# Optimization experiments

Measured on AMD Instinct MI355X. Metric: run time of the kernel, lower is better.

Reference implementation:

```python
import jax, jax.numpy as jnp
import numpy as np

D_MODEL = 1024
NUM_HEADS = 16
D_K = D_MODEL // NUM_HEADS


def setup_inputs() -> dict:
    key = jax.random.key(0)
    ks = jax.random.split(key, 9)
    s = 1.0 / np.sqrt(D_MODEL)
    inp = {
        'x': jax.random.normal(ks[0], (1, 4096, D_MODEL), dtype=jnp.float32),
        'W_q': jax.random.uniform(ks[1], (D_MODEL, D_MODEL), jnp.float32, -s, s),
        'b_q': jax.random.uniform(ks[2], (D_MODEL,), jnp.float32, -s, s),
        'W_k': jax.random.uniform(ks[3], (D_MODEL, D_MODEL), jnp.float32, -s, s),
        'b_k': jax.random.uniform(ks[4], (D_MODEL,), jnp.float32, -s, s),
        'W_v': jax.random.uniform(ks[5], (D_MODEL, D_MODEL), jnp.float32, -s, s),
        'b_v': jax.random.uniform(ks[6], (D_MODEL,), jnp.float32, -s, s),
        'W_o': jax.random.uniform(ks[7], (D_MODEL, D_MODEL), jnp.float32, -s, s),
        'b_o': jax.random.uniform(ks[8], (D_MODEL,), jnp.float32, -s, s),
    }
    return inp


def reference(x, W_q, b_q, W_k, b_k, W_v, b_v, W_o, b_o):
    B, S, _ = x.shape
    def split_heads(t):  # [B,S,D] -> [B,H,S,d_k]
        return t.reshape(B, S, NUM_HEADS, D_K).transpose(0, 2, 1, 3)
    Q = split_heads(x @ W_q + b_q)
    K = split_heads(x @ W_k + b_k)
    V = split_heads(x @ W_v + b_v)
    scale = 1.0 / jnp.sqrt(jnp.float32(D_K))
    scores = jnp.einsum('bhqd,bhkd->bhqk', Q, K) * scale  # [B,H,S,S]
    attn = jax.nn.softmax(scores, axis=-1)
    ctx = jnp.einsum('bhqk,bhkd->bhqd', attn, V)
    ctx = ctx.transpose(0, 2, 1, 3).reshape(B, S, D_MODEL)
    return ctx @ W_o + b_o
```

## Files before the change

kernel.cpp:

```cpp
#include <hip/hip_runtime.h>
#include <hip/hip_bf16.h>
#include <stdint.h>


#define DM 1024
#define SEQ 4096
#define NH 16
#define DK 64

#define QSCALE 0.18033688011112042f

typedef __attribute__((ext_vector_type(8))) short bf16x8;
typedef __attribute__((ext_vector_type(4))) float f32x4;

__device__ __forceinline__ short f2bf(float f) {
  union { float f; uint32_t u; } x; x.f = f;
  uint32_t r = x.u + 0x7fffu + ((x.u >> 16) & 1u);
  return (short)(r >> 16);
}

__device__ __forceinline__ void gl_lds16(const void* g, void* l) {
  __builtin_amdgcn_global_load_lds(
      (const __attribute__((address_space(1))) void*)g,
      (__attribute__((address_space(3))) void*)l, 16, 0, 0);
}

__global__ __launch_bounds__(256) void cvt_x_k(const float* __restrict__ in,
                                               short* __restrict__ out) {
  size_t i = (size_t)blockIdx.x * 256 + threadIdx.x;
  const float4* ip = (const float4*)in;
  float4 a = ip[2 * i], b = ip[2 * i + 1];
  bf16x8 o;
  o[0] = f2bf(a.x); o[1] = f2bf(a.y); o[2] = f2bf(a.z); o[3] = f2bf(a.w);
  o[4] = f2bf(b.x); o[5] = f2bf(b.y); o[6] = f2bf(b.z); o[7] = f2bf(b.w);
  *(bf16x8*)(out + 8 * i) = o;
}

__global__ __launch_bounds__(256) void cvt_wt_k(const float* __restrict__ W0,
                                                const float* __restrict__ W1,
                                                const float* __restrict__ W2,
                                                const float* __restrict__ W3,
                                                short* __restrict__ Wt0) {
  __shared__ alignas(16) short T[64][66];
  const int z = blockIdx.z;
  const float* W = (z == 0) ? W0 : (z == 1) ? W1 : (z == 2) ? W2 : W3;
  short* Wt = Wt0 + (size_t)z * (DM * DM);
  const int k0 = blockIdx.y * 64, n0 = blockIdx.x * 64;
#pragma unroll
  for (int rep = 0; rep < 16; ++rep) {
    int lin = rep * 256 + threadIdx.x;
    int i = lin >> 6, j = lin & 63;
    T[i][j] = f2bf(W[(size_t)(k0 + i) * DM + n0 + j]);
  }
  __syncthreads();
#pragma unroll
  for (int rep = 0; rep < 16; ++rep) {
    int lin = rep * 256 + threadIdx.x;
    int n = lin >> 6, kk = lin & 63;
    Wt[(size_t)(n0 + n) * DM + k0 + kk] = T[kk][n];
  }
}

__global__ __launch_bounds__(256) void trans_v_k(const short* __restrict__ V,
                                                 short* __restrict__ Vt) {
  __shared__ alignas(16) short T[64][66];
  const int s0 = blockIdx.x * 64, h = blockIdx.y;
#pragma unroll
  for (int rep = 0; rep < 16; ++rep) {
    int lin = rep * 256 + threadIdx.x;
    int i = lin >> 6, j = lin & 63;
    T[i][j] = V[(size_t)(s0 + i) * DM + h * DK + j];
  }
  __syncthreads();
#pragma unroll
  for (int rep = 0; rep < 16; ++rep) {
    int lin = rep * 256 + threadIdx.x;
    int d = lin >> 6, ss = lin & 63;
    Vt[((size_t)h * DK + d) * SEQ + s0 + ss] = T[ss][d];
  }
}

__global__ __launch_bounds__(256) void gemm_qkv(
    const short* __restrict__ xb, const short* __restrict__ Wt0,
    const float* __restrict__ bq, const float* __restrict__ bk,
    const float* __restrict__ bv, short* __restrict__ out0) {
  const int z = blockIdx.z;
  const short* Bt = Wt0 + (size_t)z * (DM * DM);
  const float* bias = (z == 0) ? bq : (z == 1) ? bk : bv;
  const float qs = (z == 0) ? QSCALE : 1.0f;
  short* out = out0 + (size_t)z * ((size_t)SEQ * DM);

  __shared__ alignas(16) short As[128 * 32];
  __shared__ alignas(16) short Bs[128 * 32];
  const int tid = threadIdx.x, lane = tid & 63, w = tid >> 6;
  const int bm = blockIdx.y * 128, bn = blockIdx.x * 128;
  const int wm = (w >> 1) * 64, wn = (w & 1) * 64;
  f32x4 acc[4][4] = {};

  for (int kt = 0; kt < DM; kt += 32) {
    __syncthreads();
#pragma unroll
    for (int c = 0; c < 2; ++c) {
      int i = w * 2 + c;
      int ob = i * 1024 + lane * 16;
      int row = ob >> 6, colb = ob & 63;
      gl_lds16((const char*)xb + ((size_t)(bm + row) * DM + kt) * 2 + colb,
               (char*)As + i * 1024);
      gl_lds16((const char*)Bt + ((size_t)(bn + row) * DM + kt) * 2 + colb,
               (char*)Bs + i * 1024);
    }
    __syncthreads();
    bf16x8 bfr[4];
#pragma unroll
    for (int n = 0; n < 4; ++n)
      bfr[n] = *(const bf16x8*)((const char*)Bs +
                                (wn + n * 16 + (lane & 15)) * 64 + (lane >> 4) * 16);
#pragma unroll
    for (int m = 0; m < 4; ++m) {
      bf16x8 af = *(const bf16x8*)((const char*)As +
                                   (wm + m * 16 + (lane & 15)) * 64 + (lane >> 4) * 16);
#pragma unroll
      for (int n = 0; n < 4; ++n)
        acc[m][n] = __builtin_amdgcn_mfma_f32_16x16x32_bf16(af, bfr[n], acc[m][n], 0, 0, 0);
    }
  }
  const int r0 = bm + wm + ((lane >> 4) << 2);
  const int c0 = bn + wn + (lane & 15);
#pragma unroll
  for (int n = 0; n < 4; ++n) {
    const int col = c0 + n * 16;
    const float b = bias[col];
#pragma unroll
    for (int m = 0; m < 4; ++m)
#pragma unroll
      for (int r = 0; r < 4; ++r)
        out[(size_t)(r0 + m * 16 + r) * DM + col] = f2bf((acc[m][n][r] + b) * qs);
  }
}

__global__ __launch_bounds__(256) void gemm_out(
    const short* __restrict__ A, const short* __restrict__ Bt,
    const float* __restrict__ bias, float* __restrict__ out) {
  __shared__ alignas(16) short As[128 * 32];
  __shared__ alignas(16) short Bs[128 * 32];
  const int tid = threadIdx.x, lane = tid & 63, w = tid >> 6;
  const int bm = blockIdx.y * 128, bn = blockIdx.x * 128;
  const int wm = (w >> 1) * 64, wn = (w & 1) * 64;
  f32x4 acc[4][4] = {};

  for (int kt = 0; kt < DM; kt += 32) {
    __syncthreads();
#pragma unroll
    for (int c = 0; c < 2; ++c) {
      int i = w * 2 + c;
      int ob = i * 1024 + lane * 16;
      int row = ob >> 6, colb = ob & 63;
      gl_lds16((const char*)A + ((size_t)(bm + row) * DM + kt) * 2 + colb,
               (char*)As + i * 1024);
      gl_lds16((const char*)Bt + ((size_t)(bn + row) * DM + kt) * 2 + colb,
               (char*)Bs + i * 1024);
    }
    __syncthreads();
    bf16x8 bfr[4];
#pragma unroll
    for (int n = 0; n < 4; ++n)
      bfr[n] = *(const bf16x8*)((const char*)Bs +
                                (wn + n * 16 + (lane & 15)) * 64 + (lane >> 4) * 16);
#pragma unroll
    for (int m = 0; m < 4; ++m) {
      bf16x8 af = *(const bf16x8*)((const char*)As +
                                   (wm + m * 16 + (lane & 15)) * 64 + (lane >> 4) * 16);
#pragma unroll
      for (int n = 0; n < 4; ++n)
        acc[m][n] = __builtin_amdgcn_mfma_f32_16x16x32_bf16(af, bfr[n], acc[m][n], 0, 0, 0);
    }
  }
  const int r0 = bm + wm + ((lane >> 4) << 2);
  const int c0 = bn + wn + (lane & 15);
#pragma unroll
  for (int n = 0; n < 4; ++n) {
    const int col = c0 + n * 16;
    const float b = bias[col];
#pragma unroll
    for (int m = 0; m < 4; ++m)
#pragma unroll
      for (int r = 0; r < 4; ++r)
        out[(size_t)(r0 + m * 16 + r) * DM + col] = acc[m][n][r] + b;
  }
}

__global__ __launch_bounds__(256) void attn_k(
    const short* __restrict__ Qb, const short* __restrict__ Kb,
    const short* __restrict__ Vt, short* __restrict__ ctx) {
  const int h = blockIdx.y, qt = blockIdx.x;
  const int tid = threadIdx.x, lane = tid & 63, w = tid >> 6;
  __shared__ alignas(16) short Ks[64 * 64];
  __shared__ alignas(16) short Vs[64 * 64];
  __shared__ alignas(16) short Pl[4][16 * 64];

  const int qr = qt * 64 + w * 16 + (lane & 15);
  const short* qp = Qb + (size_t)qr * DM + h * DK + ((lane >> 4) * 8);
  const bf16x8 qf0 = *(const bf16x8*)qp;
  const bf16x8 qf1 = *(const bf16x8*)(qp + 32);

  bf16x8 ones;
#pragma unroll
  for (int j = 0; j < 8; ++j) ones[j] = (short)0x3F80;

  f32x4 o[4] = {};
  f32x4 ol = {};
  float mr[4];
#pragma unroll
  for (int r = 0; r < 4; ++r) mr[r] = -1e30f;

  const int xk = (lane & 7) << 4;
  char* pbase = (char*)&Pl[w][0];
  const int q2 = (lane & 15) * 2;

  for (int s0 = 0; s0 < SEQ; s0 += 64) {
    __syncthreads();
#pragma unroll
    for (int c = 0; c < 2; ++c) {
      int i = w * 2 + c;
      int ob = i * 1024 + lane * 16;
      int row = ob >> 7, colb = ob & 127;
      int src = colb ^ ((row & 7) << 4);
      gl_lds16((const char*)Kb + ((size_t)(s0 + row) * DM + h * DK) * 2 + src,
               (char*)Ks + i * 1024);
      gl_lds16((const char*)Vt + ((size_t)(h * DK + row) * SEQ + s0) * 2 + src,
               (char*)Vs + i * 1024);
    }
    __syncthreads();

    f32x4 sc[4] = {};
    __builtin_amdgcn_s_setprio(1);
#pragma unroll
    for (int kk = 0; kk < 2; ++kk) {
      bf16x8 a = kk ? qf1 : qf0;
#pragma unroll
      for (int n = 0; n < 4; ++n) {
        bf16x8 b = *(const bf16x8*)((const char*)Ks + (n * 16 + (lane & 15)) * 128 +
                                    ((kk * 64 + (lane >> 4) * 16) ^ xk));
        sc[n] = __builtin_amdgcn_mfma_f32_16x16x32_bf16(a, b, sc[n], 0, 0, 0);
      }
    }
    __builtin_amdgcn_s_setprio(0);

    float mx[4];
#pragma unroll
    for (int r = 0; r < 4; ++r) {
      float m = fmaxf(fmaxf(sc[0][r], sc[1][r]), fmaxf(sc[2][r], sc[3][r]));
      m = fmaxf(m, __shfl_xor(m, 1));
      m = fmaxf(m, __shfl_xor(m, 2));
      m = fmaxf(m, __shfl_xor(m, 4));
      m = fmaxf(m, __shfl_xor(m, 8));
      mx[r] = m;
    }
    bool ok = (mx[0] <= mr[0] + 8.f) & (mx[1] <= mr[1] + 8.f) &
              (mx[2] <= mr[2] + 8.f) & (mx[3] <= mr[3] + 8.f);
    if (!__all(ok)) {
#pragma unroll
      for (int r = 0; r < 4; ++r) {
        float mnew = fmaxf(mr[r], mx[r]);
        float alpha = exp2f(mr[r] - mnew);
        mr[r] = mnew;
        o[0][r] *= alpha; o[1][r] *= alpha; o[2][r] *= alpha; o[3][r] *= alpha;
        ol[r] *= alpha;
      }
    }
#pragma unroll
    for (int r = 0; r < 4; ++r) {
      const int prow = (lane >> 4) * 4 + r;
      char* pr = pbase + prow * 128;
      const int X = (prow & 7) << 4;
#pragma unroll
      for (int n = 0; n < 4; ++n) {
        float p = exp2f(sc[n][r] - mr[r]);
        *(short*)(pr + ((n * 32 + q2) ^ X)) = f2bf(p);
      }
    }

    __builtin_amdgcn_s_setprio(1);
#pragma unroll
    for (int kk = 0; kk < 2; ++kk) {
      bf16x8 pa = *(const bf16x8*)(pbase + (lane & 15) * 128 +
                                   ((kk * 64 + (lane >> 4) * 16) ^ xk));
      ol = __builtin_amdgcn_mfma_f32_16x16x32_bf16(pa, ones, ol, 0, 0, 0);
#pragma unroll
      for (int n = 0; n < 4; ++n) {
        bf16x8 vb = *(const bf16x8*)((const char*)Vs + (n * 16 + (lane & 15)) * 128 +
                                     ((kk * 64 + (lane >> 4) * 16) ^ xk));
        o[n] = __builtin_amdgcn_mfma_f32_16x16x32_bf16(pa, vb, o[n], 0, 0, 0);
      }
    }
    __builtin_amdgcn_s_setprio(0);
  }

#pragma unroll
  for (int r = 0; r < 4; ++r) {
    float inv = 1.f / ol[r];
    int row = qt * 64 + w * 16 + (lane >> 4) * 4 + r;
#pragma unroll
    for (int n = 0; n < 4; ++n)
      ctx[(size_t)row * DM + h * DK + n * 16 + (lane & 15)] = f2bf(o[n][r] * inv);
  }
}

extern "C" void kernel_launch(void* const* d_in, const int* in_sizes, int n_in,
                              void* d_out, int out_size, void* d_ws, size_t ws_size,
                              hipStream_t stream) {
  const float* x  = (const float*)d_in[0];
  const float* Wq = (const float*)d_in[1];
  const float* bq = (const float*)d_in[2];
  const float* Wk = (const float*)d_in[3];
  const float* bk = (const float*)d_in[4];
  const float* Wv = (const float*)d_in[5];
  const float* bv = (const float*)d_in[6];
  const float* Wo = (const float*)d_in[7];
  const float* bo = (const float*)d_in[8];

  char* ws = (char*)d_ws;
  short* xb  = (short*)(ws + (size_t)0);
  short* Wt  = (short*)(ws + ((size_t)8 << 20));
  short* Qb  = (short*)(ws + ((size_t)16 << 20));
  short* Kb  = (short*)(ws + ((size_t)24 << 20));
  short* Vb  = (short*)(ws + ((size_t)32 << 20));
  short* Vt  = (short*)(ws + ((size_t)40 << 20));
  short* ctx = (short*)(ws + ((size_t)48 << 20));
  (void)Vb;

  cvt_x_k<<<2048, 256, 0, stream>>>(x, xb);
  cvt_wt_k<<<dim3(16, 16, 4), 256, 0, stream>>>(Wq, Wk, Wv, Wo, Wt);
  gemm_qkv<<<dim3(DM / 128, SEQ / 128, 3), 256, 0, stream>>>(xb, Wt, bq, bk, bv, Qb);
  trans_v_k<<<dim3(SEQ / 64, NH), 256, 0, stream>>>(Vb, Vt);
  attn_k<<<dim3(SEQ / 64, NH), 256, 0, stream>>>(Qb, Kb, Vt, ctx);
  gemm_out<<<dim3(DM / 128, SEQ / 128), 256, 0, stream>>>(
      ctx, Wt + (size_t)3 * (DM * DM), bo, (float*)d_out);
}
```

Measured before the change: 326.7 us.

## Double-buffer K/V tiles, pack P stores, use a single per-wave running max

The attention kernel now double-buffers the K and V tiles in LDS, issuing the next tile's global-to-LDS loads before computing on the current one, and drops one barrier per iteration. V is stored transposed with a permuted sequence order so each lane can write four probabilities at once as packed bf16 (v_cvt_pk_bf16_f32) in a single 8-byte LDS store instead of four scalar stores. The online softmax keeps one running max per wave rather than per row, which cuts the shuffle reductions. The shared max is still exact after the final normalization, but rows whose scores sit far below the wave max could underflow in exp2. Doubling the K/V buffers also raises LDS use, which may lower occupancy.

```diff
diff --git a/kernel.cpp b/kernel.cpp
--- a/kernel.cpp
+++ b/kernel.cpp
@@ -12,6 +12,7 @@
 
 typedef __attribute__((ext_vector_type(8))) short bf16x8;
 typedef __attribute__((ext_vector_type(4))) float f32x4;
+typedef __attribute__((ext_vector_type(2))) uint32_t u32x2;
 
 __device__ __forceinline__ short f2bf(float f) {
   union { float f; uint32_t u; } x; x.f = f;
@@ -76,7 +77,8 @@
   for (int rep = 0; rep < 16; ++rep) {
     int lin = rep * 256 + threadIdx.x;
     int d = lin >> 6, ss = lin & 63;
-    Vt[((size_t)h * DK + d) * SEQ + s0 + ss] = T[ss][d];
+    int sp = ((ss & 15) << 2) + (ss >> 4);
+    Vt[((size_t)h * DK + d) * SEQ + s0 + sp] = T[ss][d];
   }
 }
 
@@ -194,8 +196,8 @@
     const short* __restrict__ Vt, short* __restrict__ ctx) {
   const int h = blockIdx.y, qt = blockIdx.x;
   const int tid = threadIdx.x, lane = tid & 63, w = tid >> 6;
-  __shared__ alignas(16) short Ks[64 * 64];
-  __shared__ alignas(16) short Vs[64 * 64];
+  __shared__ alignas(16) short Ks[2][64 * 64];
+  __shared__ alignas(16) short Vs[2][64 * 64];
   __shared__ alignas(16) short Pl[4][16 * 64];
 
   const int qr = qt * 64 + w * 16 + (lane & 15);
@@ -209,16 +211,13 @@
 
   f32x4 o[4] = {};
   f32x4 ol = {};
-  float mr[4];
-#pragma unroll
-  for (int r = 0; r < 4; ++r) mr[r] = -1e30f;
+  float m = -3000.f;
 
   const int xk = (lane & 7) << 4;
   char* pbase = (char*)&Pl[w][0];
-  const int q2 = (lane & 15) * 2;
-
-  for (int s0 = 0; s0 < SEQ; s0 += 64) {
-    __syncthreads();
+  const int g = lane >> 4, cl = lane & 15;
+
+  auto stage = [&](int buf, int s0) {
 #pragma unroll
     for (int c = 0; c < 2; ++c) {
       int i = w * 2 + c;
@@ -226,11 +225,21 @@
       int row = ob >> 7, colb = ob & 127;
       int src = colb ^ ((row & 7) << 4);
       gl_lds16((const char*)Kb + ((size_t)(s0 + row) * DM + h * DK) * 2 + src,
-               (char*)Ks + i * 1024);
+               (char*)&Ks[buf][0] + i * 1024);
       gl_lds16((const char*)Vt + ((size_t)(h * DK + row) * SEQ + s0) * 2 + src,
-               (char*)Vs + i * 1024);
-    }
-    __syncthreads();
+               (char*)&Vs[buf][0] + i * 1024);
+    }
+  };
+
+  stage(0, 0);
+
+  for (int t = 0; t < SEQ / 64; ++t) {
+    const int cur = t & 1;
+    __syncthreads();
+    if (t < SEQ / 64 - 1) stage(cur ^ 1, (t + 1) * 64);
+
+    const char* kbase = (const char*)&Ks[cur][0];
+    const char* vbase = (const char*)&Vs[cur][0];
 
     f32x4 sc[4] = {};
     __builtin_amdgcn_s_setprio(1);
@@ -239,57 +248,53 @@
       bf16x8 a = kk ? qf1 : qf0;
 #pragma unroll
       for (int n = 0; n < 4; ++n) {
-        bf16x8 b = *(const bf16x8*)((const char*)Ks + (n * 16 + (lane & 15)) * 128 +
-                                    ((kk * 64 + (lane >> 4) * 16) ^ xk));
+        bf16x8 b = *(const bf16x8*)(kbase + (n * 16 + cl) * 128 +
+                                    ((kk * 64 + g * 16) ^ xk));
         sc[n] = __builtin_amdgcn_mfma_f32_16x16x32_bf16(a, b, sc[n], 0, 0, 0);
       }
     }
     __builtin_amdgcn_s_setprio(0);
 
-    float mx[4];
+    float lm = fmaxf(fmaxf(fmaxf(sc[0][0], sc[0][1]), fmaxf(sc[0][2], sc[0][3])),
+                     fmaxf(fmaxf(sc[1][0], sc[1][1]), fmaxf(sc[1][2], sc[1][3])));
+    lm = fmaxf(lm, fmaxf(fmaxf(fmaxf(sc[2][0], sc[2][1]), fmaxf(sc[2][2], sc[2][3])),
+                         fmaxf(fmaxf(sc[3][0], sc[3][1]), fmaxf(sc[3][2], sc[3][3]))));
+    lm = fmaxf(lm, __shfl_xor(lm, 1));
+    lm = fmaxf(lm, __shfl_xor(lm, 2));
+    lm = fmaxf(lm, __shfl_xor(lm, 4));
+    lm = fmaxf(lm, __shfl_xor(lm, 8));
+    if (!__all(lm <= m + 8.f)) {
+      float mn = fmaxf(m, lm);
+      float al = exp2f(m - mn);
+      m = mn;
+#pragma unroll
+      for (int n = 0; n < 4; ++n) {
+        o[n][0] *= al; o[n][1] *= al; o[n][2] *= al; o[n][3] *= al;
+      }
+      ol[0] *= al; ol[1] *= al; ol[2] *= al; ol[3] *= al;
+    }
+
 #pragma unroll
     for (int r = 0; r < 4; ++r) {
-      float m = fmaxf(fmaxf(sc[0][r], sc[1][r]), fmaxf(sc[2][r], sc[3][r]));
-      m = fmaxf(m, __shfl_xor(m, 1));
-      m = fmaxf(m, __shfl_xor(m, 2));
-      m = fmaxf(m, __shfl_xor(m, 4));
-      m = fmaxf(m, __shfl_xor(m, 8));
-      mx[r] = m;
-    }
-    bool ok = (mx[0] <= mr[0] + 8.f) & (mx[1] <= mr[1] + 8.f) &
-              (mx[2] <= mr[2] + 8.f) & (mx[3] <= mr[3] + 8.f);
-    if (!__all(ok)) {
-#pragma unroll
-      for (int r = 0; r < 4; ++r) {
-        float mnew = fmaxf(mr[r], mx[r]);
-        float alpha = exp2f(mr[r] - mnew);
-        mr[r] = mnew;
-        o[0][r] *= alpha; o[1][r] *= alpha; o[2][r] *= alpha; o[3][r] *= alpha;
-        ol[r] *= alpha;
-      }
-    }
-#pragma unroll
-    for (int r = 0; r < 4; ++r) {
-      const int prow = (lane >> 4) * 4 + r;
-      char* pr = pbase + prow * 128;
-      const int X = (prow & 7) << 4;
+      const int prow = g * 4 + r;
+      float p0 = exp2f(sc[0][r] - m), p1 = exp2f(sc[1][r] - m);
+      float p2 = exp2f(sc[2][r] - m), p3 = exp2f(sc[3][r] - m);
+      uint32_t u0, u1;
+      asm("v_cvt_pk_bf16_f32 %0, %1, %2" : "=v"(u0) : "v"(p0), "v"(p1));
+      asm("v_cvt_pk_bf16_f32 %0, %1, %2" : "=v"(u1) : "v"(p2), "v"(p3));
+      u32x2 uu; uu[0] = u0; uu[1] = u1;
+      *(u32x2*)(pbase + prow * 128 + ((cl * 8) ^ ((prow & 7) << 4))) = uu;
+    }
+
+    __builtin_amdgcn_s_setprio(1);
+#pragma unroll
+    for (int kk = 0; kk < 2; ++kk) {
+      bf16x8 pa = *(const bf16x8*)(pbase + cl * 128 + ((kk * 64 + g * 16) ^ xk));
+      ol = __builtin_amdgcn_mfma_f32_16x16x32_bf16(pa, ones, ol, 0, 0, 0);
 #pragma unroll
       for (int n = 0; n < 4; ++n) {
-        float p = exp2f(sc[n][r] - mr[r]);
-        *(short*)(pr + ((n * 32 + q2) ^ X)) = f2bf(p);
-      }
-    }
-
-    __builtin_amdgcn_s_setprio(1);
-#pragma unroll
-    for (int kk = 0; kk < 2; ++kk) {
-      bf16x8 pa = *(const bf16x8*)(pbase + (lane & 15) * 128 +
-                                   ((kk * 64 + (lane >> 4) * 16) ^ xk));
-      ol = __builtin_amdgcn_mfma_f32_16x16x32_bf16(pa, ones, ol, 0, 0, 0);
-#pragma unroll
-      for (int n = 0; n < 4; ++n) {
-        bf16x8 vb = *(const bf16x8*)((const char*)Vs + (n * 16 + (lane & 15)) * 128 +
-                                     ((kk * 64 + (lane >> 4) * 16) ^ xk));
+        bf16x8 vb = *(const bf16x8*)(vbase + (n * 16 + cl) * 128 +
+                                     ((kk * 64 + g * 16) ^ xk));
         o[n] = __builtin_amdgcn_mfma_f32_16x16x32_bf16(pa, vb, o[n], 0, 0, 0);
       }
     }
@@ -299,10 +304,10 @@
 #pragma unroll
   for (int r = 0; r < 4; ++r) {
     float inv = 1.f / ol[r];
-    int row = qt * 64 + w * 16 + (lane >> 4) * 4 + r;
+    int row = qt * 64 + w * 16 + g * 4 + r;
 #pragma unroll
     for (int n = 0; n < 4; ++n)
-      ctx[(size_t)row * DM + h * DK + n * 16 + (lane & 15)] = f2bf(o[n][r] * inv);
+      ctx[(size_t)row * DM + h * DK + n * 16 + cl] = f2bf(o[n][r] * inv);
   }
 }
 
@@ -327,7 +332,6 @@
   short* Vb  = (short*)(ws + ((size_t)32 << 20));
   short* Vt  = (short*)(ws + ((size_t)40 << 20));
   short* ctx = (short*)(ws + ((size_t)48 << 20));
-  (void)Vb;
 
   cvt_x_k<<<2048, 256, 0, stream>>>(x, xb);
   cvt_wt_k<<<dim3(16, 16, 4), 256, 0, stream>>>(Wq, Wk, Wv, Wo, Wt);
```

New measurement: 291.4 us. 10.8% less time.
